# Kernel tuning notes

Hardware: AMD Instinct MI355X
Metric: run time of the kernel (lower is better)

Reference implementation:

```python
import jax, jax.numpy as jnp
import numpy as np

NQ, NKV, D = 32, 8, 64
HID = 2048
EPS = 1e-5
THETA = 1000000.0


def _rmsnorm(x, w):
    var = jnp.mean(x * x, axis=-1, keepdims=True)
    return x * jax.lax.rsqrt(var + EPS) * w


def setup_inputs() -> dict:
    key = jax.random.key(0)
    k1, k2, k3 = jax.random.split(key, 3)
    T = 2048
    positions = jnp.arange(T, dtype=jnp.int64) if jax.config.jax_enable_x64 else jnp.arange(T, dtype=jnp.int32)
    hidden_states = jax.random.normal(k1, (T, HID), dtype=jnp.float32)
    w_qkv = jax.random.normal(k2, (HID, (NQ + 2 * NKV) * D), dtype=jnp.float32) / np.sqrt(HID)
    w_out = jax.random.normal(k3, (NQ * D, HID), dtype=jnp.float32) / np.sqrt(NQ * D)
    q_ln_w = jnp.ones((D,), dtype=jnp.float32)
    k_ln_w = jnp.ones((D,), dtype=jnp.float32)
    return {"positions": positions, "hidden_states": hidden_states, "w_qkv": w_qkv,
            "w_out": w_out, "q_ln_w": q_ln_w, "k_ln_w": k_ln_w}


def reference(positions, hidden_states, w_qkv, w_out, q_ln_w, k_ln_w):
    T = hidden_states.shape[0]
    qkv = hidden_states @ w_qkv  # [T, (NQ+2*NKV)*D]
    q = qkv[:, : NQ * D].reshape(T, NQ, D)
    k = qkv[:, NQ * D : (NQ + NKV) * D].reshape(T, NKV, D)
    v = qkv[:, (NQ + NKV) * D :].reshape(T, NKV, D)
    # per-head RMSNorm on q and k
    q = _rmsnorm(q, q_ln_w)
    k = _rmsnorm(k, k_ln_w)
    # neox-style RoPE (rotate halves)
    inv_freq = 1.0 / (THETA ** (jnp.arange(0, D, 2, dtype=jnp.float32) / D))
    ang = positions.astype(jnp.float32)[:, None] * inv_freq  # [T, D/2]
    cos = jnp.cos(ang)[:, None, :]
    sin = jnp.sin(ang)[:, None, :]
    def rope(x):
        x1, x2 = x[..., : D // 2], x[..., D // 2 :]
        return jnp.concatenate([x1 * cos - x2 * sin, x2 * cos + x1 * sin], axis=-1)
    q = rope(q)
    k = rope(k)
    # grouped-query causal attention (one sequence, positions define order)
    G = NQ // NKV
    qg = q.reshape(T, NKV, G, D)
    scores = jnp.einsum('tkgd,skd->kgts', qg, k) * (D ** -0.5)  # [NKV,G,T,T]
    causal = jnp.arange(T)[:, None] >= jnp.arange(T)[None, :]
    scores = jnp.where(causal[None, None], scores, -1e30)
    probs = jax.nn.softmax(scores, axis=-1)
    attn = jnp.einsum('kgts,skd->tkgd', probs, v).reshape(T, NQ * D)
    return attn @ w_out
```

## Files before the change

kernel.cpp:

```cpp
#include <hip/hip_runtime.h>

typedef __bf16 bhalf;
typedef __bf16 bhalf8 __attribute__((ext_vector_type(8)));
typedef __bf16 bhalf4 __attribute__((ext_vector_type(4)));
typedef float f32x4 __attribute__((ext_vector_type(4)));

typedef __attribute__((address_space(1))) const void* gas_p;
typedef __attribute__((address_space(3))) void* las_p;

#define T_SEQ 2048
#define HIDN  2048
#define NQH   32
#define NKVH  8
#define DH    64
#define NQKV  3072

__global__ __launch_bounds__(256) void cast_bf16_k(const float* __restrict__ in,
                                                   bhalf* __restrict__ out, int n) {
  int i = (blockIdx.x * 256 + threadIdx.x) * 4;
  if (i + 3 < n) {
    float4 v = *(const float4*)(in + i);
    bhalf4 o;
    o[0] = (bhalf)v.x; o[1] = (bhalf)v.y; o[2] = (bhalf)v.z; o[3] = (bhalf)v.w;
    *(bhalf4*)(out + i) = o;
  }
}

__global__ __launch_bounds__(256) void transpose_cast_k(const float* __restrict__ in,
                                                        bhalf* __restrict__ out, int R, int C) {
  __shared__ float tile[32][33];
  int bx = blockIdx.x * 32;
  int by = blockIdx.y * 32;
  int tx = threadIdx.x & 31, ty = threadIdx.x >> 5;
#pragma unroll
  for (int p = 0; p < 4; ++p)
    tile[ty + 8 * p][tx] = in[(size_t)(by + ty + 8 * p) * C + bx + tx];
  __syncthreads();
#pragma unroll
  for (int p = 0; p < 4; ++p)
    out[(size_t)(bx + ty + 8 * p) * R + by + tx] = (bhalf)tile[tx][ty + 8 * p];
}

__global__ __launch_bounds__(256) void transpose_bf16_k(const bhalf* __restrict__ in,
                                                        bhalf* __restrict__ out, int R, int C) {
  __shared__ bhalf tile[32][33];
  int bx = blockIdx.x * 32;
  int by = blockIdx.y * 32;
  int tx = threadIdx.x & 31, ty = threadIdx.x >> 5;
#pragma unroll
  for (int p = 0; p < 4; ++p)
    tile[ty + 8 * p][tx] = in[(size_t)(by + ty + 8 * p) * C + bx + tx];
  __syncthreads();
#pragma unroll
  for (int p = 0; p < 4; ++p)
    out[(size_t)(bx + ty + 8 * p) * R + by + tx] = tile[tx][ty + 8 * p];
}

__device__ __forceinline__ void gemm_core(const bhalf* __restrict__ A,
                                          const bhalf* __restrict__ Bt, int K,
                                          int bm, int bn, int tid,
                                          bhalf* As, bhalf* Bs, f32x4 acc[2][4]) {
  int lane = tid & 63, wv = tid >> 6;
  int m16 = lane & 15, q4 = lane >> 4;
  int srow = tid >> 3;
  int scol = ((tid & 7) ^ (srow & 7)) * 8;
  const bhalf* asrc = A + (size_t)(bm + srow) * K + scol;
  const bhalf* bsrc = Bt + (size_t)(bn + srow) * K + scol;
  bhalf* adst = As + (wv * 8) * 64;
  bhalf* bdst = Bs + (wv * 8) * 64;
  int swz = m16 & 7;

  for (int k0 = 0; k0 < K; k0 += 64) {
#pragma unroll
    for (int c = 0; c < 4; ++c)
      __builtin_amdgcn_global_load_lds((gas_p)(asrc + (size_t)(c * 32) * K + k0),
                                       (las_p)(adst + c * 2048), 16, 0, 0);
#pragma unroll
    for (int c = 0; c < 2; ++c)
      __builtin_amdgcn_global_load_lds((gas_p)(bsrc + (size_t)(c * 32) * K + k0),
                                       (las_p)(bdst + c * 2048), 16, 0, 0);
    __syncthreads();
    bhalf8 af[2][2], bf[4][2];
#pragma unroll
    for (int mi = 0; mi < 2; ++mi)
#pragma unroll
      for (int ks = 0; ks < 2; ++ks)
        af[mi][ks] = *(const bhalf8*)&As[(wv * 32 + mi * 16 + m16) * 64 +
                                         (((ks * 4 + q4) ^ swz) * 8)];
#pragma unroll
    for (int ni = 0; ni < 4; ++ni)
#pragma unroll
      for (int ks = 0; ks < 2; ++ks)
        bf[ni][ks] = *(const bhalf8*)&Bs[(ni * 16 + m16) * 64 +
                                         (((ks * 4 + q4) ^ swz) * 8)];
#pragma unroll
    for (int mi = 0; mi < 2; ++mi)
#pragma unroll
      for (int ni = 0; ni < 4; ++ni) {
        acc[mi][ni] = __builtin_amdgcn_mfma_f32_16x16x32_bf16(af[mi][0], bf[ni][0], acc[mi][ni], 0, 0, 0);
        acc[mi][ni] = __builtin_amdgcn_mfma_f32_16x16x32_bf16(af[mi][1], bf[ni][1], acc[mi][ni], 0, 0, 0);
      }
    __syncthreads();
  }
}

__global__ __launch_bounds__(256) void gemm1_fused_k(const bhalf* __restrict__ A,
                                                     const bhalf* __restrict__ Bt,
                                                     const int* __restrict__ pos,
                                                     const float* __restrict__ qw,
                                                     const float* __restrict__ kw,
                                                     bhalf* __restrict__ qo,
                                                     bhalf* __restrict__ ko,
                                                     bhalf* __restrict__ vo) {
  __shared__ __align__(16) bhalf As[128 * 64];
  __shared__ __align__(16) bhalf Bs[64 * 64];
  int tid = threadIdx.x, lane = tid & 63, wv = tid >> 6;
  int m16 = lane & 15, q4 = lane >> 4;
  int bm = blockIdx.y * 128, bn = blockIdx.x * 64, h = blockIdx.x;
  f32x4 zero4 = {0.f, 0.f, 0.f, 0.f};
  f32x4 acc[2][4];
#pragma unroll
  for (int mi = 0; mi < 2; ++mi)
#pragma unroll
    for (int ni = 0; ni < 4; ++ni) acc[mi][ni] = zero4;

  gemm_core(A, Bt, HIDN, bm, bn, tid, As, Bs, acc);

  int wr0 = wv * 32;
  if (h < 40) {
    float wd[4];
    const float* wptr = (h < 32) ? qw : kw;
#pragma unroll
    for (int ni = 0; ni < 4; ++ni) wd[ni] = wptr[ni * 16 + m16];
    float f0 = exp2f((float)m16 * -0.6228615177913804f);
    float f1 = f0 * 0.001f;
#pragma unroll
    for (int mi = 0; mi < 2; ++mi)
#pragma unroll
      for (int r = 0; r < 4; ++r) {
        int trow = bm + wr0 + mi * 16 + q4 * 4 + r;
        float x0 = acc[mi][0][r], x1 = acc[mi][1][r], x2 = acc[mi][2][r], x3 = acc[mi][3][r];
        float ss = x0 * x0 + x1 * x1 + x2 * x2 + x3 * x3;
        ss += __shfl_xor(ss, 1);
        ss += __shfl_xor(ss, 2);
        ss += __shfl_xor(ss, 4);
        ss += __shfl_xor(ss, 8);
        float sc = rsqrtf(ss * (1.0f / 64.0f) + 1e-5f);
        float y0 = x0 * sc * wd[0], y1 = x1 * sc * wd[1];
        float y2 = x2 * sc * wd[2], y3 = x3 * sc * wd[3];
        float p = (float)pos[trow];
        float a0 = p * f0, a1 = p * f1;
        float c0 = cosf(a0), s0 = sinf(a0), c1 = cosf(a1), s1 = sinf(a1);
        float o0 = y0 * c0 - y2 * s0, o2 = y2 * c0 + y0 * s0;
        float o1 = y1 * c1 - y3 * s1, o3 = y3 * c1 + y1 * s1;
        bhalf* dst = (h < 32) ? (qo + (size_t)trow * 2048 + h * 64 + m16)
                              : (ko + (size_t)trow * 512 + (h - 32) * 64 + m16);
        dst[0] = (bhalf)o0; dst[16] = (bhalf)o1; dst[32] = (bhalf)o2; dst[48] = (bhalf)o3;
      }
  } else {
#pragma unroll
    for (int mi = 0; mi < 2; ++mi)
#pragma unroll
      for (int r = 0; r < 4; ++r) {
        int trow = bm + wr0 + mi * 16 + q4 * 4 + r;
        bhalf* dst = vo + (size_t)trow * 512 + (h - 40) * 64 + m16;
        dst[0] = (bhalf)acc[mi][0][r]; dst[16] = (bhalf)acc[mi][1][r];
        dst[32] = (bhalf)acc[mi][2][r]; dst[48] = (bhalf)acc[mi][3][r];
      }
  }
}

__global__ __launch_bounds__(256) void gemm2_k(const bhalf* __restrict__ A,
                                               const bhalf* __restrict__ Bt,
                                               float* __restrict__ C) {
  __shared__ __align__(16) bhalf As[128 * 64];
  __shared__ __align__(16) bhalf Bs[64 * 64];
  int tid = threadIdx.x, lane = tid & 63, wv = tid >> 6;
  int m16 = lane & 15, q4 = lane >> 4;
  int bm = blockIdx.y * 128, bn = blockIdx.x * 64;
  f32x4 zero4 = {0.f, 0.f, 0.f, 0.f};
  f32x4 acc[2][4];
#pragma unroll
  for (int mi = 0; mi < 2; ++mi)
#pragma unroll
    for (int ni = 0; ni < 4; ++ni) acc[mi][ni] = zero4;

  gemm_core(A, Bt, HIDN, bm, bn, tid, As, Bs, acc);

  int wr0 = wv * 32;
#pragma unroll
  for (int mi = 0; mi < 2; ++mi)
#pragma unroll
    for (int r = 0; r < 4; ++r) {
      size_t base = (size_t)(bm + wr0 + mi * 16 + q4 * 4 + r) * 2048 + bn + m16;
      C[base] = acc[mi][0][r]; C[base + 16] = acc[mi][1][r];
      C[base + 32] = acc[mi][2][r]; C[base + 48] = acc[mi][3][r];
    }
}

__global__ __launch_bounds__(256) void attn_k(const bhalf* __restrict__ q,
                                              const bhalf* __restrict__ k,
                                              const bhalf* __restrict__ vt,
                                              bhalf* __restrict__ o) {
  __shared__ __align__(16) bhalf Kb[2][4096];
  __shared__ __align__(16) bhalf Vb[2][4096];
  __shared__ __align__(16) bhalf Pb[4][16][72];
  int tid = threadIdx.x, lane = tid & 63, w = tid >> 6;
  int h = blockIdx.x, kh = h >> 2;
  int qt = 31 - blockIdx.y;
  int qb = qt * 64;
  int m16 = lane & 15, q4 = lane >> 4;
  int wrow0 = qb + w * 16;

  const float C1 = 0.18033688011112042f;
  const float C2 = 11.541560327111707f;

  const bhalf* qp = q + (size_t)(wrow0 + m16) * 2048 + h * 64;
  bhalf8 qf0 = *(const bhalf8*)(qp + q4 * 8);
  bhalf8 qf1 = *(const bhalf8*)(qp + 32 + q4 * 8);

  int srow = tid >> 3;
  int scol = ((tid & 7) ^ (srow & 7)) * 8;
  const bhalf* ksrc = k + (size_t)srow * 512 + kh * 64 + scol;
  const bhalf* vsrc = vt + (size_t)(kh * 64 + srow) * 2048 + scol;
  bhalf* kdst = &Kb[0][0] + w * 512;
  bhalf* vdst = &Vb[0][0] + w * 512;

  auto stage = [&](int c) {
    int buf = c & 1, s0 = c * 64;
#pragma unroll
    for (int j = 0; j < 2; ++j) {
      __builtin_amdgcn_global_load_lds((gas_p)(ksrc + (size_t)(s0 + j * 32) * 512),
                                       (las_p)(kdst + buf * 4096 + j * 2048), 16, 0, 0);
      __builtin_amdgcn_global_load_lds((gas_p)(vsrc + (size_t)(j * 32) * 2048 + s0),
                                       (las_p)(vdst + buf * 4096 + j * 2048), 16, 0, 0);
    }
  };

  f32x4 zero4 = {0.f, 0.f, 0.f, 0.f};
  f32x4 oac[4];
  float psum[4] = {0.f, 0.f, 0.f, 0.f};
#pragma unroll
  for (int ni = 0; ni < 4; ++ni) oac[ni] = zero4;
  int swz = m16 & 7;

  stage(0);
  for (int c = 0; c <= qt; ++c) {
    __syncthreads();
    if (c < qt) stage(c + 1);
    int buf = c & 1, s0 = c * 64;
    if (c < qt) {
      bhalf8 kf[4][2];
#pragma unroll
      for (int st = 0; st < 4; ++st)
#pragma unroll
        for (int ks = 0; ks < 2; ++ks)
          kf[st][ks] = *(const bhalf8*)&Kb[buf][(st * 16 + m16) * 64 + (((ks * 4 + q4) ^ swz) * 8)];
      f32x4 sv[4];
#pragma unroll
      for (int st = 0; st < 4; ++st) {
        f32x4 t0 = __builtin_amdgcn_mfma_f32_16x16x32_bf16(qf0, kf[st][0], zero4, 0, 0, 0);
        sv[st] = __builtin_amdgcn_mfma_f32_16x16x32_bf16(qf1, kf[st][1], t0, 0, 0, 0);
      }
#pragma unroll
      for (int st = 0; st < 4; ++st)
#pragma unroll
        for (int r = 0; r < 4; ++r) {
          float pe = exp2f(sv[st][r] * C1 - C2);
          psum[r] += pe;
          Pb[w][q4 * 4 + r][st * 16 + m16] = (bhalf)pe;
        }
      bhalf8 vf[4][2];
#pragma unroll
      for (int ni = 0; ni < 4; ++ni)
#pragma unroll
        for (int ks = 0; ks < 2; ++ks)
          vf[ni][ks] = *(const bhalf8*)&Vb[buf][(ni * 16 + m16) * 64 + (((ks * 4 + q4) ^ swz) * 8)];
      bhalf8 ap0 = *(const bhalf8*)&Pb[w][m16][q4 * 8];
      bhalf8 ap1 = *(const bhalf8*)&Pb[w][m16][32 + q4 * 8];
#pragma unroll
      for (int ni = 0; ni < 4; ++ni) {
        oac[ni] = __builtin_amdgcn_mfma_f32_16x16x32_bf16(ap0, vf[ni][0], oac[ni], 0, 0, 0);
        oac[ni] = __builtin_amdgcn_mfma_f32_16x16x32_bf16(ap1, vf[ni][1], oac[ni], 0, 0, 0);
      }
    } else {
      bhalf8 kf[4][2];
      f32x4 sv[4];
#pragma unroll
      for (int st = 0; st < 4; ++st)
        if (st <= w) {
#pragma unroll
          for (int ks = 0; ks < 2; ++ks)
            kf[st][ks] = *(const bhalf8*)&Kb[buf][(st * 16 + m16) * 64 + (((ks * 4 + q4) ^ swz) * 8)];
          f32x4 t0 = __builtin_amdgcn_mfma_f32_16x16x32_bf16(qf0, kf[st][0], zero4, 0, 0, 0);
          sv[st] = __builtin_amdgcn_mfma_f32_16x16x32_bf16(qf1, kf[st][1], t0, 0, 0, 0);
        }
      int stwr = (w >= 2) ? 3 : 1;
#pragma unroll
      for (int st = 0; st < 4; ++st) {
        if (st > stwr) continue;
#pragma unroll
        for (int r = 0; r < 4; ++r) {
          float pe = 0.f;
          if (st <= w) {
            int trow = wrow0 + q4 * 4 + r;
            int col = s0 + st * 16 + m16;
            pe = (col <= trow) ? exp2f(sv[st][r] * C1 - C2) : 0.f;
          }
          psum[r] += pe;
          Pb[w][q4 * 4 + r][st * 16 + m16] = (bhalf)pe;
        }
      }
      int ksmax = (w >= 2) ? 1 : 0;
      bhalf8 vf[4][2];
#pragma unroll
      for (int ni = 0; ni < 4; ++ni)
#pragma unroll
        for (int ks = 0; ks < 2; ++ks)
          if (ks <= ksmax)
            vf[ni][ks] = *(const bhalf8*)&Vb[buf][(ni * 16 + m16) * 64 + (((ks * 4 + q4) ^ swz) * 8)];
      bhalf8 ap0 = *(const bhalf8*)&Pb[w][m16][q4 * 8];
#pragma unroll
      for (int ni = 0; ni < 4; ++ni)
        oac[ni] = __builtin_amdgcn_mfma_f32_16x16x32_bf16(ap0, vf[ni][0], oac[ni], 0, 0, 0);
      if (ksmax) {
        bhalf8 ap1 = *(const bhalf8*)&Pb[w][m16][32 + q4 * 8];
#pragma unroll
        for (int ni = 0; ni < 4; ++ni)
          oac[ni] = __builtin_amdgcn_mfma_f32_16x16x32_bf16(ap1, vf[ni][1], oac[ni], 0, 0, 0);
      }
    }
  }
#pragma unroll
  for (int r = 0; r < 4; ++r) {
    float ps = psum[r];
    ps += __shfl_xor(ps, 1);
    ps += __shfl_xor(ps, 2);
    ps += __shfl_xor(ps, 4);
    ps += __shfl_xor(ps, 8);
    psum[r] = 1.0f / ps;
  }
#pragma unroll
  for (int ni = 0; ni < 4; ++ni)
#pragma unroll
    for (int r = 0; r < 4; ++r) {
      int trow = wrow0 + q4 * 4 + r;
      o[(size_t)trow * 2048 + h * 64 + ni * 16 + m16] = (bhalf)(oac[ni][r] * psum[r]);
    }
}

extern "C" void kernel_launch(void* const* d_in, const int* in_sizes, int n_in,
                              void* d_out, int out_size, void* d_ws, size_t ws_size,
                              hipStream_t stream) {
  const int* positions = (const int*)d_in[0];
  const float* hidden  = (const float*)d_in[1];
  const float* w_qkv   = (const float*)d_in[2];
  const float* w_out   = (const float*)d_in[3];
  const float* q_ln    = (const float*)d_in[4];
  const float* k_ln    = (const float*)d_in[5];
  float* out = (float*)d_out;

  char* wsp = (char*)d_ws;
  bhalf* hid_bf  = (bhalf*)(wsp);
  bhalf* wqkvT   = (bhalf*)(wsp + 8388608);
  bhalf* woutT   = (bhalf*)(wsp + 20971520);
  bhalf* q_bf    = (bhalf*)(wsp + 29360128);
  bhalf* k_bf    = (bhalf*)(wsp + 37748736);
  bhalf* v_bf    = (bhalf*)(wsp + 39845888);
  bhalf* vt_g    = (bhalf*)(wsp + 41943040);
  bhalf* attn_bf = (bhalf*)(wsp + 44040192);

  cast_bf16_k<<<T_SEQ * HIDN / 1024, 256, 0, stream>>>(hidden, hid_bf, T_SEQ * HIDN);
  transpose_cast_k<<<dim3(NQKV / 32, HIDN / 32), 256, 0, stream>>>(w_qkv, wqkvT, HIDN, NQKV);
  transpose_cast_k<<<dim3(HIDN / 32, HIDN / 32), 256, 0, stream>>>(w_out, woutT, HIDN, HIDN);
  gemm1_fused_k<<<dim3(NQKV / 64, T_SEQ / 128), 256, 0, stream>>>(
      hid_bf, wqkvT, positions, q_ln, k_ln, q_bf, k_bf, v_bf);
  transpose_bf16_k<<<dim3(512 / 32, T_SEQ / 32), 256, 0, stream>>>(v_bf, vt_g, T_SEQ, 512);
  attn_k<<<dim3(NQH, 32), 256, 0, stream>>>(q_bf, k_bf, vt_g, attn_bf);
  gemm2_k<<<dim3(HIDN / 64, T_SEQ / 128), 256, 0, stream>>>(attn_bf, woutT, out);
}
```

Before: 224.6 us.

## Double-buffer GEMM LDS tiles and transpose attention score MFMA for packed P writes

The shared GEMM core now uses two LDS buffers and prefetches the next K tile before computing the current one, dropping the trailing barrier so loads overlap compute. The attention kernel swaps the MFMA operands to produce transposed score tiles. Each lane then holds four consecutive key columns for one query row, so P can be written to LDS as packed 4-element vectors and the row sum reduces across fewer shuffles. It also adds s_setprio around MFMA bursts and simplifies the diagonal causal mask. The trade-offs are doubled LDS per GEMM block, which may cut occupancy, and extra shuffles to redistribute the inverse row sums.

```diff
diff --git a/kernel.cpp b/kernel.cpp
--- a/kernel.cpp
+++ b/kernel.cpp
@@ -70,28 +70,36 @@
   bhalf* bdst = Bs + (wv * 8) * 64;
   int swz = m16 & 7;
 
-  for (int k0 = 0; k0 < K; k0 += 64) {
+  auto stage = [&](int k0, int sbuf) {
 #pragma unroll
     for (int c = 0; c < 4; ++c)
       __builtin_amdgcn_global_load_lds((gas_p)(asrc + (size_t)(c * 32) * K + k0),
-                                       (las_p)(adst + c * 2048), 16, 0, 0);
+                                       (las_p)(adst + sbuf * 8192 + c * 2048), 16, 0, 0);
 #pragma unroll
     for (int c = 0; c < 2; ++c)
       __builtin_amdgcn_global_load_lds((gas_p)(bsrc + (size_t)(c * 32) * K + k0),
-                                       (las_p)(bdst + c * 2048), 16, 0, 0);
+                                       (las_p)(bdst + sbuf * 4096 + c * 2048), 16, 0, 0);
+  };
+
+  stage(0, 0);
+  int buf = 0;
+  for (int k0 = 0; k0 < K; k0 += 64) {
     __syncthreads();
+    if (k0 + 64 < K) stage(k0 + 64, buf ^ 1);
+    const bhalf* Ab = As + buf * 8192;
+    const bhalf* Bb = Bs + buf * 4096;
     bhalf8 af[2][2], bf[4][2];
 #pragma unroll
     for (int mi = 0; mi < 2; ++mi)
 #pragma unroll
       for (int ks = 0; ks < 2; ++ks)
-        af[mi][ks] = *(const bhalf8*)&As[(wv * 32 + mi * 16 + m16) * 64 +
+        af[mi][ks] = *(const bhalf8*)&Ab[(wv * 32 + mi * 16 + m16) * 64 +
                                          (((ks * 4 + q4) ^ swz) * 8)];
 #pragma unroll
     for (int ni = 0; ni < 4; ++ni)
 #pragma unroll
       for (int ks = 0; ks < 2; ++ks)
-        bf[ni][ks] = *(const bhalf8*)&Bs[(ni * 16 + m16) * 64 +
+        bf[ni][ks] = *(const bhalf8*)&Bb[(ni * 16 + m16) * 64 +
                                          (((ks * 4 + q4) ^ swz) * 8)];
 #pragma unroll
     for (int mi = 0; mi < 2; ++mi)
@@ -100,7 +108,7 @@
         acc[mi][ni] = __builtin_amdgcn_mfma_f32_16x16x32_bf16(af[mi][0], bf[ni][0], acc[mi][ni], 0, 0, 0);
         acc[mi][ni] = __builtin_amdgcn_mfma_f32_16x16x32_bf16(af[mi][1], bf[ni][1], acc[mi][ni], 0, 0, 0);
       }
-    __syncthreads();
+    buf ^= 1;
   }
 }
 
@@ -112,8 +120,8 @@
                                                      bhalf* __restrict__ qo,
                                                      bhalf* __restrict__ ko,
                                                      bhalf* __restrict__ vo) {
-  __shared__ __align__(16) bhalf As[128 * 64];
-  __shared__ __align__(16) bhalf Bs[64 * 64];
+  __shared__ __align__(16) bhalf As[2 * 128 * 64];
+  __shared__ __align__(16) bhalf Bs[2 * 64 * 64];
   int tid = threadIdx.x, lane = tid & 63, wv = tid >> 6;
   int m16 = lane & 15, q4 = lane >> 4;
   int bm = blockIdx.y * 128, bn = blockIdx.x * 64, h = blockIdx.x;
@@ -173,8 +181,8 @@
 __global__ __launch_bounds__(256) void gemm2_k(const bhalf* __restrict__ A,
                                                const bhalf* __restrict__ Bt,
                                                float* __restrict__ C) {
-  __shared__ __align__(16) bhalf As[128 * 64];
-  __shared__ __align__(16) bhalf Bs[64 * 64];
+  __shared__ __align__(16) bhalf As[2 * 128 * 64];
+  __shared__ __align__(16) bhalf Bs[2 * 64 * 64];
   int tid = threadIdx.x, lane = tid & 63, wv = tid >> 6;
   int m16 = lane & 15, q4 = lane >> 4;
   int bm = blockIdx.y * 128, bn = blockIdx.x * 64;
@@ -239,10 +247,12 @@
 
   f32x4 zero4 = {0.f, 0.f, 0.f, 0.f};
   f32x4 oac[4];
-  float psum[4] = {0.f, 0.f, 0.f, 0.f};
+  float psum = 0.f;
 #pragma unroll
   for (int ni = 0; ni < 4; ++ni) oac[ni] = zero4;
   int swz = m16 & 7;
+  bhalf* pwr = &Pb[w][m16][q4 * 4];
+  const bhalf* par = &Pb[w][m16][q4 * 8];
 
   stage(0);
   for (int c = 0; c <= qt; ++c) {
@@ -257,32 +267,39 @@
         for (int ks = 0; ks < 2; ++ks)
           kf[st][ks] = *(const bhalf8*)&Kb[buf][(st * 16 + m16) * 64 + (((ks * 4 + q4) ^ swz) * 8)];
       f32x4 sv[4];
+      __builtin_amdgcn_s_setprio(1);
 #pragma unroll
       for (int st = 0; st < 4; ++st) {
-        f32x4 t0 = __builtin_amdgcn_mfma_f32_16x16x32_bf16(qf0, kf[st][0], zero4, 0, 0, 0);
-        sv[st] = __builtin_amdgcn_mfma_f32_16x16x32_bf16(qf1, kf[st][1], t0, 0, 0, 0);
-      }
-#pragma unroll
-      for (int st = 0; st < 4; ++st)
+        f32x4 t0 = __builtin_amdgcn_mfma_f32_16x16x32_bf16(kf[st][0], qf0, zero4, 0, 0, 0);
+        sv[st] = __builtin_amdgcn_mfma_f32_16x16x32_bf16(kf[st][1], qf1, t0, 0, 0, 0);
+      }
+      __builtin_amdgcn_s_setprio(0);
+#pragma unroll
+      for (int st = 0; st < 4; ++st) {
+        bhalf4 pk;
 #pragma unroll
         for (int r = 0; r < 4; ++r) {
           float pe = exp2f(sv[st][r] * C1 - C2);
-          psum[r] += pe;
-          Pb[w][q4 * 4 + r][st * 16 + m16] = (bhalf)pe;
+          psum += pe;
+          pk[r] = (bhalf)pe;
         }
+        *(bhalf4*)(pwr + st * 16) = pk;
+      }
       bhalf8 vf[4][2];
 #pragma unroll
       for (int ni = 0; ni < 4; ++ni)
 #pragma unroll
         for (int ks = 0; ks < 2; ++ks)
           vf[ni][ks] = *(const bhalf8*)&Vb[buf][(ni * 16 + m16) * 64 + (((ks * 4 + q4) ^ swz) * 8)];
-      bhalf8 ap0 = *(const bhalf8*)&Pb[w][m16][q4 * 8];
-      bhalf8 ap1 = *(const bhalf8*)&Pb[w][m16][32 + q4 * 8];
+      bhalf8 ap0 = *(const bhalf8*)par;
+      bhalf8 ap1 = *(const bhalf8*)(par + 32);
+      __builtin_amdgcn_s_setprio(1);
 #pragma unroll
       for (int ni = 0; ni < 4; ++ni) {
         oac[ni] = __builtin_amdgcn_mfma_f32_16x16x32_bf16(ap0, vf[ni][0], oac[ni], 0, 0, 0);
         oac[ni] = __builtin_amdgcn_mfma_f32_16x16x32_bf16(ap1, vf[ni][1], oac[ni], 0, 0, 0);
       }
+      __builtin_amdgcn_s_setprio(0);
     } else {
       bhalf8 kf[4][2];
       f32x4 sv[4];
@@ -292,24 +309,26 @@
 #pragma unroll
           for (int ks = 0; ks < 2; ++ks)
             kf[st][ks] = *(const bhalf8*)&Kb[buf][(st * 16 + m16) * 64 + (((ks * 4 + q4) ^ swz) * 8)];
-          f32x4 t0 = __builtin_amdgcn_mfma_f32_16x16x32_bf16(qf0, kf[st][0], zero4, 0, 0, 0);
-          sv[st] = __builtin_amdgcn_mfma_f32_16x16x32_bf16(qf1, kf[st][1], t0, 0, 0, 0);
+          f32x4 t0 = __builtin_amdgcn_mfma_f32_16x16x32_bf16(kf[st][0], qf0, zero4, 0, 0, 0);
+          sv[st] = __builtin_amdgcn_mfma_f32_16x16x32_bf16(kf[st][1], qf1, t0, 0, 0, 0);
         }
       int stwr = (w >= 2) ? 3 : 1;
 #pragma unroll
       for (int st = 0; st < 4; ++st) {
         if (st > stwr) continue;
+        bhalf4 pk;
 #pragma unroll
         for (int r = 0; r < 4; ++r) {
           float pe = 0.f;
-          if (st <= w) {
-            int trow = wrow0 + q4 * 4 + r;
-            int col = s0 + st * 16 + m16;
-            pe = (col <= trow) ? exp2f(sv[st][r] * C1 - C2) : 0.f;
+          if (st < w) {
+            pe = exp2f(sv[st][r] * C1 - C2);
+          } else if (st == w) {
+            pe = (q4 * 4 + r <= m16) ? exp2f(sv[st][r] * C1 - C2) : 0.f;
           }
-          psum[r] += pe;
-          Pb[w][q4 * 4 + r][st * 16 + m16] = (bhalf)pe;
+          psum += pe;
+          pk[r] = (bhalf)pe;
         }
+        *(bhalf4*)(pwr + st * 16) = pk;
       }
       int ksmax = (w >= 2) ? 1 : 0;
       bhalf8 vf[4][2];
@@ -319,33 +338,30 @@
         for (int ks = 0; ks < 2; ++ks)
           if (ks <= ksmax)
             vf[ni][ks] = *(const bhalf8*)&Vb[buf][(ni * 16 + m16) * 64 + (((ks * 4 + q4) ^ swz) * 8)];
-      bhalf8 ap0 = *(const bhalf8*)&Pb[w][m16][q4 * 8];
+      bhalf8 ap0 = *(const bhalf8*)par;
 #pragma unroll
       for (int ni = 0; ni < 4; ++ni)
         oac[ni] = __builtin_amdgcn_mfma_f32_16x16x32_bf16(ap0, vf[ni][0], oac[ni], 0, 0, 0);
       if (ksmax) {
-        bhalf8 ap1 = *(const bhalf8*)&Pb[w][m16][32 + q4 * 8];
+        bhalf8 ap1 = *(const bhalf8*)(par + 32);
 #pragma unroll
         for (int ni = 0; ni < 4; ++ni)
           oac[ni] = __builtin_amdgcn_mfma_f32_16x16x32_bf16(ap1, vf[ni][1], oac[ni], 0, 0, 0);
       }
     }
   }
-#pragma unroll
-  for (int r = 0; r < 4; ++r) {
-    float ps = psum[r];
-    ps += __shfl_xor(ps, 1);
-    ps += __shfl_xor(ps, 2);
-    ps += __shfl_xor(ps, 4);
-    ps += __shfl_xor(ps, 8);
-    psum[r] = 1.0f / ps;
-  }
+  psum += __shfl_xor(psum, 16);
+  psum += __shfl_xor(psum, 32);
+  float inv = 1.0f / psum;
+  float invr[4];
+#pragma unroll
+  for (int r = 0; r < 4; ++r) invr[r] = __shfl(inv, q4 * 4 + r);
 #pragma unroll
   for (int ni = 0; ni < 4; ++ni)
 #pragma unroll
     for (int r = 0; r < 4; ++r) {
       int trow = wrow0 + q4 * 4 + r;
-      o[(size_t)trow * 2048 + h * 64 + ni * 16 + m16] = (bhalf)(oac[ni][r] * psum[r]);
+      o[(size_t)trow * 2048 + h * 64 + ni * 16 + m16] = (bhalf)(oac[ni][r] * invr[r]);
     }
 }
 
```

Measured after the change: 222.0 us. Within noise of the previous version (-1.2%).
